# Kernel tuning notes

Measured on AMD Instinct MI355X. Metric: run time of the kernel, lower is better.

## Reference

```python
import jax, jax.numpy as jnp
import numpy as np

N_NODES = 50000
N_EDGES = 800000
STATE_DIM = 128
H1 = 96
H2 = 64


def setup_inputs() -> dict:
    key = jax.random.key(0)
    ks = jax.random.split(key, 10)
    x = jax.random.normal(ks[0], (N_NODES, STATE_DIM), dtype=jnp.float32)
    edge_index = jax.random.randint(ks[1], (2, N_EDGES), 0, N_NODES, dtype=jnp.int64)
    # GCNConv weight [in, out] and bias
    W1 = jax.random.normal(ks[2], (STATE_DIM, H1), dtype=jnp.float32) / np.sqrt(STATE_DIM)
    b1 = jnp.zeros((H1,), dtype=jnp.float32)
    lw1 = jax.random.normal(ks[3], (H1, H1), dtype=jnp.float32) / np.sqrt(H1)
    lb1 = jax.random.normal(ks[4], (H1,), dtype=jnp.float32) * 0.01
    lw2 = jax.random.normal(ks[5], (H1, H2), dtype=jnp.float32) / np.sqrt(H1)
    lb2 = jax.random.normal(ks[6], (H2,), dtype=jnp.float32) * 0.01
    lw3 = jax.random.normal(ks[7], (H2, 1), dtype=jnp.float32) / np.sqrt(H2)
    lb3 = jax.random.normal(ks[8], (1,), dtype=jnp.float32) * 0.01
    return {"x": x, "edge_index": edge_index, "W1": W1, "b1": b1,
            "lw1": lw1, "lb1": lb1, "lw2": lw2, "lb2": lb2, "lw3": lw3, "lb3": lb3}


def reference(x, edge_index, W1, b1, lw1, lb1, lw2, lb2, lw3, lb3):
    N = x.shape[0]
    loop = jnp.arange(N, dtype=edge_index.dtype)
    src = jnp.concatenate([edge_index[0], loop])
    dst = jnp.concatenate([edge_index[1], loop])
    deg = jax.ops.segment_sum(jnp.ones_like(dst, dtype=x.dtype), dst, num_segments=N)
    dinv = jnp.where(deg > 0, jax.lax.rsqrt(jnp.maximum(deg, 1.0)), 0.0)
    norm = dinv[src] * dinv[dst]  # [E+N]
    h = x @ W1  # [N, H1] transform before propagation
    agg = jax.ops.segment_sum(h[src] * norm[:, None], dst, num_segments=N) + b1
    out = jax.nn.relu(agg)            # [N, H1]
    g = jnp.sum(out, axis=0)          # sum pooling over nodes -> [H1]
    g = jax.nn.relu(g @ lw1 + lb1)
    g = jax.nn.relu(g @ lw2 + lb2)
    return g @ lw3 + lb3              # [1]
```

## Files before the change

kernel.cpp:

```cpp
#include <hip/hip_runtime.h>
#include <stdint.h>

#define N_NODES 50000
#define N_EDGES 800000
#define D_IN 128
#define H1 96
#define H2 64
#define GEMM_NODES 32
#define GEMM_BLOCKS ((N_NODES + GEMM_NODES - 1) / GEMM_NODES)
#define COUNT_BLOCKS 256
#define SCAN_BLK 256
#define N_SBLK ((N_NODES + SCAN_BLK - 1) / SCAN_BLK)
#define SCAT_BLOCKS 2048
#define SCALE_BLOCKS 512

__global__ __launch_bounds__(256) void k1_gemm_count(const float* __restrict__ x,
                                                     const float* __restrict__ W1,
                                                     float* __restrict__ h,
                                                     const int* __restrict__ dst,
                                                     int* __restrict__ deg) {
    __shared__ float sW[D_IN * H1];
    __shared__ float sx[GEMM_NODES * D_IN];
    int tid = threadIdx.x;

    if (blockIdx.x < GEMM_BLOCKS) {
        for (int i = tid; i < D_IN * H1 / 4; i += 256)
            ((float4*)sW)[i] = ((const float4*)W1)[i];

        int base = blockIdx.x * GEMM_NODES;
        const float4* x4 = (const float4*)x;
        for (int i = tid; i < GEMM_NODES * D_IN / 4; i += 256) {
            int n = base + i / (D_IN / 4);
            if (n < N_NODES) ((float4*)sx)[i] = x4[(size_t)base * (D_IN / 4) + i];
        }
        __syncthreads();

        int fg = tid & 31;
        int ng = tid >> 5;

        float acc[4][3];
#pragma unroll
        for (int i = 0; i < 4; ++i)
#pragma unroll
            for (int j = 0; j < 3; ++j) acc[i][j] = 0.0f;

#pragma unroll 4
        for (int k = 0; k < D_IN; ++k) {
            float w0 = sW[k * H1 + fg];
            float w1 = sW[k * H1 + fg + 32];
            float w2 = sW[k * H1 + fg + 64];
#pragma unroll
            for (int i = 0; i < 4; ++i) {
                float xv = sx[(ng * 4 + i) * D_IN + k];
                acc[i][0] = fmaf(xv, w0, acc[i][0]);
                acc[i][1] = fmaf(xv, w1, acc[i][1]);
                acc[i][2] = fmaf(xv, w2, acc[i][2]);
            }
        }

#pragma unroll
        for (int i = 0; i < 4; ++i) {
            int n = base + ng * 4 + i;
            if (n < N_NODES) {
                h[(size_t)n * H1 + fg]      = acc[i][0];
                h[(size_t)n * H1 + fg + 32] = acc[i][1];
                h[(size_t)n * H1 + fg + 64] = acc[i][2];
            }
        }
    } else {
        int bid = blockIdx.x - GEMM_BLOCKS;
        int gid = bid * 256 + tid;
        int stride = COUNT_BLOCKS * 256;
        const int4* d4 = (const int4*)dst;
        for (int i = gid; i < N_EDGES / 4; i += stride) {
            int4 d = d4[i];
            atomicAdd(&deg[d.x], 1);
            atomicAdd(&deg[d.y], 1);
            atomicAdd(&deg[d.z], 1);
            atomicAdd(&deg[d.w], 1);
        }
    }
}

__global__ __launch_bounds__(SCAN_BLK) void deg_part_kernel(const int* __restrict__ deg,
                                                            int* __restrict__ block_sums) {
    __shared__ int s[SCAN_BLK];
    int t = threadIdx.x;
    int i = blockIdx.x * SCAN_BLK + t;
    s[t] = (i < N_NODES) ? deg[i] : 0;
    __syncthreads();
    for (int off = SCAN_BLK / 2; off > 0; off >>= 1) {
        if (t < off) s[t] += s[t + off];
        __syncthreads();
    }
    if (t == 0) block_sums[blockIdx.x] = s[0];
}

__global__ __launch_bounds__(SCAN_BLK) void block_scan_kernel(int* __restrict__ block_sums) {
    __shared__ int s[SCAN_BLK];
    int t = threadIdx.x;
    int v = (t < N_SBLK) ? block_sums[t] : 0;
    s[t] = v;
    __syncthreads();
    for (int off = 1; off < SCAN_BLK; off <<= 1) {
        int u = (t >= off) ? s[t - off] : 0;
        __syncthreads();
        s[t] += u;
        __syncthreads();
    }
    if (t < N_SBLK) block_sums[t] = s[t] - v;
}

__global__ __launch_bounds__(SCAN_BLK) void deg_scan_kernel(const int* __restrict__ deg,
                                                            const int* __restrict__ block_off,
                                                            int* __restrict__ row_start,
                                                            int* __restrict__ cursor,
                                                            float* __restrict__ dinv) {
    __shared__ int s[SCAN_BLK];
    int t = threadIdx.x;
    int i = blockIdx.x * SCAN_BLK + t;
    int v = (i < N_NODES) ? deg[i] : 0;
    s[t] = v;
    __syncthreads();
    for (int off = 1; off < SCAN_BLK; off <<= 1) {
        int u = (t >= off) ? s[t - off] : 0;
        __syncthreads();
        s[t] += u;
        __syncthreads();
    }
    int excl = s[t] - v + block_off[blockIdx.x];
    if (i < N_NODES) {
        row_start[i] = excl;
        cursor[i] = excl;
        dinv[i] = rsqrtf((float)v + 1.0f);
    }
    if (i == 0) row_start[N_NODES] = N_EDGES;
}

__global__ __launch_bounds__(256) void k3_scatter_scale(const int* __restrict__ src,
                                                        const int* __restrict__ dst,
                                                        int* __restrict__ cursor,
                                                        int* __restrict__ sorted_src,
                                                        float* __restrict__ h,
                                                        const float* __restrict__ dinv) {
    int tid = threadIdx.x;
    if (blockIdx.x < SCAT_BLOCKS) {
        int gid = blockIdx.x * 256 + tid;
        int stride = SCAT_BLOCKS * 256;
        for (int e = gid; e < N_EDGES; e += stride) {
            int d = dst[e];
            int pos = atomicAdd(&cursor[d], 1);
            sorted_src[pos] = src[e];
        }
    } else {
        int bid = blockIdx.x - SCAT_BLOCKS;
        int gid = bid * 256 + tid;
        int stride = SCALE_BLOCKS * 256;
        float4* h4 = (float4*)h;
        const int TOT = N_NODES * (H1 / 4);
        for (int i = gid; i < TOT; i += stride) {
            int n = i / (H1 / 4);
            float dv = dinv[n];
            float4 v = h4[i];
            v.x *= dv; v.y *= dv; v.z *= dv; v.w *= dv;
            h4[i] = v;
        }
    }
}

__global__ __launch_bounds__(256) void agg_pool_kernel(const float* __restrict__ hs,
                                                       const int* __restrict__ row_start,
                                                       const int* __restrict__ sorted_src,
                                                       const float* __restrict__ dinv,
                                                       const float* __restrict__ b1,
                                                       float* __restrict__ g) {
    int tid = threadIdx.x;
    int grp = tid >> 7;
    int f = tid & 127;
    bool act = f < H1;
    float bf = act ? b1[f] : 0.0f;
    float gacc = 0.0f;

    for (int n = blockIdx.x * 2 + grp; n < N_NODES; n += gridDim.x * 2) {
        float acc = act ? hs[(size_t)n * H1 + f] : 0.0f;
        int e = row_start[n];
        int eend = row_start[n + 1];
        for (; e + 4 <= eend; e += 4) {
            int s0 = sorted_src[e];
            int s1 = sorted_src[e + 1];
            int s2 = sorted_src[e + 2];
            int s3 = sorted_src[e + 3];
            if (act) {
                float v0 = hs[(size_t)s0 * H1 + f];
                float v1 = hs[(size_t)s1 * H1 + f];
                float v2 = hs[(size_t)s2 * H1 + f];
                float v3 = hs[(size_t)s3 * H1 + f];
                acc += (v0 + v1) + (v2 + v3);
            }
        }
        for (; e < eend; ++e) {
            int s = sorted_src[e];
            if (act) acc += hs[(size_t)s * H1 + f];
        }
        if (act) gacc += fmaxf(fmaf(dinv[n], acc, bf), 0.0f);
    }

    __shared__ float sg[H1];
    if (grp == 0 && act) sg[f] = gacc;
    __syncthreads();
    if (grp == 1 && act) atomicAdd(&sg[f], gacc);
    __syncthreads();
    if (grp == 0 && act) atomicAdd(&g[f], sg[f]);
}

__global__ __launch_bounds__(256) void mlp_kernel(const float* __restrict__ g,
                           const float* __restrict__ lw1, const float* __restrict__ lb1,
                           const float* __restrict__ lw2, const float* __restrict__ lb2,
                           const float* __restrict__ lw3, const float* __restrict__ lb3,
                           float* __restrict__ out) {
    __shared__ float slw1[H1 * H1];
    __shared__ float slw2[H1 * H2];
    __shared__ float slw3[H2];
    __shared__ float sg[H1], v1[H1], v2[H2];
    int t = threadIdx.x;
    for (int i = t; i < H1 * H1 / 4; i += 256)
        ((float4*)slw1)[i] = ((const float4*)lw1)[i];
    for (int i = t; i < H1 * H2 / 4; i += 256)
        ((float4*)slw2)[i] = ((const float4*)lw2)[i];
    if (t < H2) slw3[t] = lw3[t];
    if (t < H1) sg[t] = g[t];
    __syncthreads();
    if (t < H1) {
        float a = lb1[t];
#pragma unroll 8
        for (int k = 0; k < H1; ++k) a = fmaf(sg[k], slw1[k * H1 + t], a);
        v1[t] = fmaxf(a, 0.0f);
    }
    __syncthreads();
    if (t < H2) {
        float a = lb2[t];
#pragma unroll 8
        for (int k = 0; k < H1; ++k) a = fmaf(v1[k], slw2[k * H2 + t], a);
        v2[t] = fmaxf(a, 0.0f);
    }
    __syncthreads();
    if (t == 0) {
        float a = lb3[0];
#pragma unroll 8
        for (int k = 0; k < H2; ++k) a = fmaf(v2[k], slw3[k], a);
        out[0] = a;
    }
}

extern "C" void kernel_launch(void* const* d_in, const int* in_sizes, int n_in,
                              void* d_out, int out_size, void* d_ws, size_t ws_size,
                              hipStream_t stream) {
    const float* x   = (const float*)d_in[0];
    const int*   ei  = (const int*)d_in[1];
    const float* W1  = (const float*)d_in[2];
    const float* b1  = (const float*)d_in[3];
    const float* lw1 = (const float*)d_in[4];
    const float* lb1 = (const float*)d_in[5];
    const float* lw2 = (const float*)d_in[6];
    const float* lb2 = (const float*)d_in[7];
    const float* lw3 = (const float*)d_in[8];
    const float* lb3 = (const float*)d_in[9];
    float* out = (float*)d_out;

    const int* src = ei;
    const int* dst = ei + N_EDGES;

    char* ws = (char*)d_ws;
    size_t off = 0;
    auto alloc = [&](size_t bytes) {
        char* p = ws + off;
        off = (off + bytes + 255) & ~(size_t)255;
        return p;
    };
    int*   deg        = (int*)alloc((size_t)N_NODES * sizeof(int));
    float* g          = (float*)alloc((size_t)H1 * sizeof(float));
    float* dinv       = (float*)alloc((size_t)N_NODES * sizeof(float));
    int*   row_start  = (int*)alloc((size_t)(N_NODES + 1) * sizeof(int));
    int*   cursor     = (int*)alloc((size_t)N_NODES * sizeof(int));
    int*   block_sums = (int*)alloc((size_t)N_SBLK * sizeof(int));
    int*   sorted_src = (int*)alloc((size_t)N_EDGES * sizeof(int));
    float* h          = (float*)alloc((size_t)N_NODES * H1 * sizeof(float));
    (void)ws_size;

    hipMemsetAsync(deg, 0, (char*)(g + H1) - (char*)deg, stream);

    k1_gemm_count<<<GEMM_BLOCKS + COUNT_BLOCKS, 256, 0, stream>>>(x, W1, h, dst, deg);

    deg_part_kernel<<<N_SBLK, SCAN_BLK, 0, stream>>>(deg, block_sums);
    block_scan_kernel<<<1, SCAN_BLK, 0, stream>>>(block_sums);
    deg_scan_kernel<<<N_SBLK, SCAN_BLK, 0, stream>>>(deg, block_sums, row_start, cursor, dinv);

    k3_scatter_scale<<<SCAT_BLOCKS + SCALE_BLOCKS, 256, 0, stream>>>(src, dst, cursor, sorted_src, h, dinv);

    agg_pool_kernel<<<2048, 256, 0, stream>>>(h, row_start, sorted_src, dinv, b1, g);

    mlp_kernel<<<1, 256, 0, stream>>>(g, lw1, lb1, lw2, lb2, lw3, lb3, out);
}
```

Before: 248.3 us.

## Drop shared W1 staging, vectorize edge scatter, split aggregation into three launches

The GEMM now reads W1 straight from global memory and no longer stages it in shared memory. This lowers LDS use per block and may allow more blocks per CU. The edge scatter loads src and dst as int4 and writes the sorted entries with nontemporal stores. The count-block count is doubled, and the aggregation runs as three launches over node thirds, which adds launch overhead and reduces parallelism per launch. Global W1 reads rely on the cache and may cost more than LDS reads.

```diff
diff --git a/kernel.cpp b/kernel.cpp
--- a/kernel.cpp
+++ b/kernel.cpp
@@ -8,25 +8,22 @@
 #define H2 64
 #define GEMM_NODES 32
 #define GEMM_BLOCKS ((N_NODES + GEMM_NODES - 1) / GEMM_NODES)
-#define COUNT_BLOCKS 256
+#define COUNT_BLOCKS 512
 #define SCAN_BLK 256
 #define N_SBLK ((N_NODES + SCAN_BLK - 1) / SCAN_BLK)
 #define SCAT_BLOCKS 2048
-#define SCALE_BLOCKS 512
+#define AGG_BLOCKS 2048
+#define N_THIRD 16667
 
 __global__ __launch_bounds__(256) void k1_gemm_count(const float* __restrict__ x,
                                                      const float* __restrict__ W1,
                                                      float* __restrict__ h,
                                                      const int* __restrict__ dst,
                                                      int* __restrict__ deg) {
-    __shared__ float sW[D_IN * H1];
     __shared__ float sx[GEMM_NODES * D_IN];
     int tid = threadIdx.x;
 
     if (blockIdx.x < GEMM_BLOCKS) {
-        for (int i = tid; i < D_IN * H1 / 4; i += 256)
-            ((float4*)sW)[i] = ((const float4*)W1)[i];
-
         int base = blockIdx.x * GEMM_NODES;
         const float4* x4 = (const float4*)x;
         for (int i = tid; i < GEMM_NODES * D_IN / 4; i += 256) {
@@ -46,9 +43,9 @@
 
 #pragma unroll 4
         for (int k = 0; k < D_IN; ++k) {
-            float w0 = sW[k * H1 + fg];
-            float w1 = sW[k * H1 + fg + 32];
-            float w2 = sW[k * H1 + fg + 64];
+            float w0 = W1[k * H1 + fg];
+            float w1 = W1[k * H1 + fg + 32];
+            float w2 = W1[k * H1 + fg + 64];
 #pragma unroll
             for (int i = 0; i < 4; ++i) {
                 float xv = sx[(ng * 4 + i) * D_IN + k];
@@ -147,15 +144,24 @@
     if (blockIdx.x < SCAT_BLOCKS) {
         int gid = blockIdx.x * 256 + tid;
         int stride = SCAT_BLOCKS * 256;
-        for (int e = gid; e < N_EDGES; e += stride) {
-            int d = dst[e];
-            int pos = atomicAdd(&cursor[d], 1);
-            sorted_src[pos] = src[e];
+        const int4* s4p = (const int4*)src;
+        const int4* d4p = (const int4*)dst;
+        for (int i = gid; i < N_EDGES / 4; i += stride) {
+            int4 sv = s4p[i];
+            int4 dv = d4p[i];
+            int p0 = atomicAdd(&cursor[dv.x], 1);
+            int p1 = atomicAdd(&cursor[dv.y], 1);
+            int p2 = atomicAdd(&cursor[dv.z], 1);
+            int p3 = atomicAdd(&cursor[dv.w], 1);
+            __builtin_nontemporal_store(sv.x, &sorted_src[p0]);
+            __builtin_nontemporal_store(sv.y, &sorted_src[p1]);
+            __builtin_nontemporal_store(sv.z, &sorted_src[p2]);
+            __builtin_nontemporal_store(sv.w, &sorted_src[p3]);
         }
     } else {
         int bid = blockIdx.x - SCAT_BLOCKS;
         int gid = bid * 256 + tid;
-        int stride = SCALE_BLOCKS * 256;
+        int stride = 512 * 256;
         float4* h4 = (float4*)h;
         const int TOT = N_NODES * (H1 / 4);
         for (int i = gid; i < TOT; i += stride) {
@@ -173,7 +179,8 @@
                                                        const int* __restrict__ sorted_src,
                                                        const float* __restrict__ dinv,
                                                        const float* __restrict__ b1,
-                                                       float* __restrict__ g) {
+                                                       float* __restrict__ g,
+                                                       int n0, int n1) {
     int tid = threadIdx.x;
     int grp = tid >> 7;
     int f = tid & 127;
@@ -181,7 +188,7 @@
     float bf = act ? b1[f] : 0.0f;
     float gacc = 0.0f;
 
-    for (int n = blockIdx.x * 2 + grp; n < N_NODES; n += gridDim.x * 2) {
+    for (int n = n0 + blockIdx.x * 2 + grp; n < n1; n += gridDim.x * 2) {
         float acc = act ? hs[(size_t)n * H1 + f] : 0.0f;
         int e = row_start[n];
         int eend = row_start[n + 1];
@@ -295,9 +302,14 @@
     block_scan_kernel<<<1, SCAN_BLK, 0, stream>>>(block_sums);
     deg_scan_kernel<<<N_SBLK, SCAN_BLK, 0, stream>>>(deg, block_sums, row_start, cursor, dinv);
 
-    k3_scatter_scale<<<SCAT_BLOCKS + SCALE_BLOCKS, 256, 0, stream>>>(src, dst, cursor, sorted_src, h, dinv);
-
-    agg_pool_kernel<<<2048, 256, 0, stream>>>(h, row_start, sorted_src, dinv, b1, g);
+    k3_scatter_scale<<<SCAT_BLOCKS + 512, 256, 0, stream>>>(src, dst, cursor, sorted_src, h, dinv);
+
+    agg_pool_kernel<<<AGG_BLOCKS, 256, 0, stream>>>(h, row_start, sorted_src, dinv, b1, g,
+                                                    0, N_THIRD);
+    agg_pool_kernel<<<AGG_BLOCKS, 256, 0, stream>>>(h, row_start, sorted_src, dinv, b1, g,
+                                                    N_THIRD, 2 * N_THIRD);
+    agg_pool_kernel<<<AGG_BLOCKS, 256, 0, stream>>>(h, row_start, sorted_src, dinv, b1, g,
+                                                    2 * N_THIRD, N_NODES);
 
     mlp_kernel<<<1, 256, 0, stream>>>(g, lw1, lb1, lw2, lb2, lw3, lb3, out);
 }
```

After: 364.2 us. 46.6% more time.
